# Performance work log

Measured on AMD Instinct MI355X. Metric: run time of the kernel, lower is better.

## Reference

```python
import jax, jax.numpy as jnp
import numpy as np

ALPHA = 0.2  # LeakyReLU negative slope


def setup_inputs() -> dict:
    key = jax.random.key(0)
    k1, k2, k3 = jax.random.split(key, 3)
    B, N, IN, OUT = 64, 2048, 1024, 1024
    features = jax.random.normal(k1, (B, N, IN), dtype=jnp.float32)
    # Xavier-uniform-ish scaling for weights
    W = jax.random.normal(k2, (OUT, IN), dtype=jnp.float32) * (1.0 / np.sqrt(IN))
    w_b = jnp.zeros((OUT,), dtype=jnp.float32)
    a_w = jax.random.normal(k3, (2 * OUT,), dtype=jnp.float32) * (1.0 / np.sqrt(2 * OUT))
    a_b = jnp.zeros((), dtype=jnp.float32)
    bias_out = jnp.zeros((OUT,), dtype=jnp.float32)
    return {"features": features, "W": W, "w_b": w_b, "a_w": a_w, "a_b": a_b, "bias_out": bias_out}


def reference(features, W, w_b, a_w, a_b, bias_out):
    # h = Linear(in_dim, out_dim)(features): [B, N, D]
    h = jnp.einsum('bni,di->bnd', features, W) + w_b
    D = h.shape[-1]
    a1, a2 = a_w[:D], a_w[D:]
    # concat([h_expand, h]) @ a == h[:, :1] . a1 + h . a2  (h_expand broadcasts node 0)
    e = (h[:, 0:1, :] @ a1[:, None]) + jnp.einsum('bnd,d->bn', h, a2)[..., None] + a_b  # [B, N, 1]
    e = jnp.where(e >= 0, e, ALPHA * e)  # LeakyReLU
    attention = jax.nn.softmax(e, axis=1)  # softmax over nodes, [B, N, 1]
    # dropout p=0.0 -> identity
    pooled = jnp.einsum('bnk,bnd->bkd', attention, h)  # [B, 1, D]
    return jax.nn.relu(pooled + bias_out)
```

## Files before the change

kernel.cpp:

```cpp
#include <hip/hip_runtime.h>

#define ALPHA 0.2f
constexpr int B_   = 64;
constexpr int N_   = 2048;
constexpr int IN_  = 1024;
constexpr int OUT_ = 1024;
constexpr int CHUNK = 256;
constexpr int NCH   = N_ / CHUNK;
constexpr int RPW   = CHUNK / 4;

constexpr size_t WA1   = 0;
constexpr size_t WA2   = 1024;
constexpr size_t E0    = 2048;
constexpr size_t ZPART = 2112;
constexpr size_t PART1 = 4096;
constexpr size_t PART2 = 135168;
constexpr size_t GPART = 266240;
constexpr size_t GV    = 790528;

__device__ inline float wave_reduce_sum(float v) {
    #pragma unroll
    for (int off = 32; off > 0; off >>= 1) v += __shfl_xor(v, off);
    return v;
}

__global__ void kW(const float* __restrict__ W, const float* __restrict__ aw,
                   float* __restrict__ ws) {
    int t = threadIdx.x, blk = blockIdx.x;
    float4 acc1 = make_float4(0.f, 0.f, 0.f, 0.f);
    float4 acc2 = make_float4(0.f, 0.f, 0.f, 0.f);
    #pragma unroll
    for (int r = 0; r < 8; ++r) {
        int d = blk * 8 + r;
        float a1 = aw[d], a2 = aw[OUT_ + d];
        float4 w = ((const float4*)(W + (size_t)d * IN_))[t];
        acc1.x += a1 * w.x; acc1.y += a1 * w.y; acc1.z += a1 * w.z; acc1.w += a1 * w.w;
        acc2.x += a2 * w.x; acc2.y += a2 * w.y; acc2.z += a2 * w.z; acc2.w += a2 * w.w;
    }
    ((float4*)(ws + PART1))[blk * 256 + t] = acc1;
    ((float4*)(ws + PART2))[blk * 256 + t] = acc2;
}

__global__ void kS(const float* __restrict__ f, const float* __restrict__ wb,
                   const float* __restrict__ aw, float* __restrict__ ws) {
    int t = threadIdx.x;
    if (blockIdx.x < 8) {
        int idx = blockIdx.x * 256 + t;
        int which = idx >> 10, col = idx & 1023;
        const float* p = ws + (which ? PART2 : PART1) + col;
        float s = 0.f;
        #pragma unroll 8
        for (int r = 0; r < 128; ++r) s += p[(size_t)r * 1024];
        ws[(which ? WA2 : WA1) + col] = s;
    } else {
        int b = blockIdx.x - 8;
        float4 fv = ((const float4*)(f + (size_t)b * N_ * IN_))[t];
        const float4* p1 = (const float4*)(ws + PART1);
        float acc = 0.f;
        #pragma unroll 8
        for (int r = 0; r < 128; ++r) {
            float4 p = p1[(size_t)r * 256 + t];
            acc += fv.x * p.x + fv.y * p.y + fv.z * p.z + fv.w * p.w;
        }
        float4 wbv = ((const float4*)wb)[t];
        float4 a1v = ((const float4*)aw)[t];
        float4 a2v = ((const float4*)(aw + OUT_))[t];
        acc += wbv.x * (a1v.x + a2v.x) + wbv.y * (a1v.y + a2v.y)
             + wbv.z * (a1v.z + a2v.z) + wbv.w * (a1v.w + a2v.w);
        __shared__ float red[256];
        red[t] = acc;
        __syncthreads();
        for (int off = 128; off > 0; off >>= 1) {
            if (t < off) red[t] += red[t + off];
            __syncthreads();
        }
        if (t == 0) ws[E0 + b] = red[0];
    }
}

__global__ void kMain(const float* __restrict__ f, const float* __restrict__ ab,
                      float* __restrict__ ws) {
    int b = blockIdx.y, chunk = blockIdx.x;
    int t = threadIdx.x, wave = t >> 6, lane = t & 63;
    float cst = ws[E0 + b] + ab[0];

    const float4* wa2_4 = (const float4*)(ws + WA2);
    float4 ra2[4];
    #pragma unroll
    for (int k = 0; k < 4; ++k) ra2[k] = wa2_4[k * 64 + lane];

    const float4* fbase = (const float4*)(f + ((size_t)b * N_ + (size_t)chunk * CHUNK) * IN_);
    float4 acc[4];
    #pragma unroll
    for (int k = 0; k < 4; ++k) acc[k] = make_float4(0.f, 0.f, 0.f, 0.f);
    float z = 0.f;

    float4 v[4], nv[4];
    int r = wave;
    #pragma unroll
    for (int k = 0; k < 4; ++k) v[k] = fbase[(size_t)r * 256 + k * 64 + lane];

    for (int i = 0; i < RPW; ++i) {
        int rn = r + 4;
        if (i + 1 < RPW) {
            #pragma unroll
            for (int k = 0; k < 4; ++k) nv[k] = fbase[(size_t)rn * 256 + k * 64 + lane];
        }
        float dot = 0.f;
        #pragma unroll
        for (int k = 0; k < 4; ++k)
            dot += v[k].x * ra2[k].x + v[k].y * ra2[k].y + v[k].z * ra2[k].z + v[k].w * ra2[k].w;
        dot = wave_reduce_sum(dot);
        float e = dot + cst;
        e = e >= 0.f ? e : ALPHA * e;
        float w = __expf(e);
        z += w;
        #pragma unroll
        for (int k = 0; k < 4; ++k) {
            acc[k].x += w * v[k].x; acc[k].y += w * v[k].y;
            acc[k].z += w * v[k].z; acc[k].w += w * v[k].w;
        }
        if (i + 1 < RPW) {
            #pragma unroll
            for (int k = 0; k < 4; ++k) v[k] = nv[k];
        }
        r = rn;
    }

    __shared__ float4 gbuf[4][256];
    __shared__ float  zbuf[4];
    #pragma unroll
    for (int k = 0; k < 4; ++k) gbuf[wave][k * 64 + lane] = acc[k];
    if (lane == 0) zbuf[wave] = z;
    __syncthreads();
    float4 s0 = gbuf[0][t], s1 = gbuf[1][t], s2 = gbuf[2][t], s3 = gbuf[3][t];
    float4 s = make_float4(s0.x + s1.x + s2.x + s3.x, s0.y + s1.y + s2.y + s3.y,
                           s0.z + s1.z + s2.z + s3.z, s0.w + s1.w + s2.w + s3.w);
    ((float4*)(ws + GPART))[((size_t)b * NCH + chunk) * 256 + t] = s;
    if (t == 0) ws[ZPART + b * NCH + chunk] = zbuf[0] + zbuf[1] + zbuf[2] + zbuf[3];
}

__global__ void kE(float* __restrict__ ws) {
    int b = blockIdx.x, t = threadIdx.x;
    __shared__ float zinv;
    if (t == 0) {
        float zz = 0.f;
        #pragma unroll
        for (int c = 0; c < NCH; ++c) zz += ws[ZPART + b * NCH + c];
        zinv = 1.0f / zz;
    }
    __syncthreads();
    const float4* gp = (const float4*)(ws + GPART);
    float4 acc = make_float4(0.f, 0.f, 0.f, 0.f);
    #pragma unroll
    for (int c = 0; c < NCH; ++c) {
        float4 v = gp[((size_t)b * NCH + c) * 256 + t];
        acc.x += v.x; acc.y += v.y; acc.z += v.z; acc.w += v.w;
    }
    acc.x *= zinv; acc.y *= zinv; acc.z *= zinv; acc.w *= zinv;
    ((float4*)(ws + GV))[b * 256 + t] = acc;
}

__global__ void kF(const float* __restrict__ W, const float* __restrict__ wb,
                   const float* __restrict__ bias, const float* __restrict__ ws,
                   float* __restrict__ out) {
    int t = threadIdx.x, wave = t >> 6, lane = t & 63;
    int d  = blockIdx.x * 4 + wave;
    int b0 = blockIdx.y * 32;
    const float4* w4 = (const float4*)(W + (size_t)d * IN_);
    float4 wreg[4];
    #pragma unroll
    for (int k = 0; k < 4; ++k) wreg[k] = w4[k * 64 + lane];
    float wbb = wb[d] + bias[d];
    const float4* gv = (const float4*)(ws + GV);
    #pragma unroll 4
    for (int bi = 0; bi < 32; ++bi) {
        int b = b0 + bi;
        float acc = 0.f;
        #pragma unroll
        for (int k = 0; k < 4; ++k) {
            float4 g = gv[b * 256 + k * 64 + lane];
            acc += g.x * wreg[k].x + g.y * wreg[k].y + g.z * wreg[k].z + g.w * wreg[k].w;
        }
        acc = wave_reduce_sum(acc);
        if (lane == 0) {
            float p = acc + wbb;
            out[(size_t)b * OUT_ + d] = p > 0.f ? p : 0.f;
        }
    }
}

extern "C" void kernel_launch(void* const* d_in, const int* in_sizes, int n_in,
                              void* d_out, int out_size, void* d_ws, size_t ws_size,
                              hipStream_t stream) {
    const float* f    = (const float*)d_in[0];
    const float* W    = (const float*)d_in[1];
    const float* wb   = (const float*)d_in[2];
    const float* aw   = (const float*)d_in[3];
    const float* ab   = (const float*)d_in[4];
    const float* bias = (const float*)d_in[5];
    float* out = (float*)d_out;
    float* ws  = (float*)d_ws;

    kW   <<<dim3(128), 256, 0, stream>>>(W, aw, ws);
    kS   <<<dim3(8 + B_), 256, 0, stream>>>(f, wb, aw, ws);
    kMain<<<dim3(NCH, B_), 256, 0, stream>>>(f, ab, ws);
    kE   <<<dim3(B_), 256, 0, stream>>>(ws);
    kF   <<<dim3(OUT_ / 4, 2), 256, 0, stream>>>(W, wb, bias, ws, out);
}
```

Measured before the change: 129.8 us.

## Fuse W·a projection and node-0 score precompute into one column-split kernel

Replaces the two preprocessing kernels (partial W^T a reductions, then a cross-block sum plus node-0 dot) with a single kernel where each of 64 blocks owns 16 input columns. Each block fully reduces W^T a1 and W^T a2 for its columns and writes partial node-0 scores per batch. The main kernel now sums those 64 partials itself at startup. This removes one launch and the large partial-sum workspace round trip. In exchange, W is read with narrow strided column accesses, and every main-kernel block does a small extra reduction plus a barrier.

```diff
diff --git a/kernel.cpp b/kernel.cpp
--- a/kernel.cpp
+++ b/kernel.cpp
@@ -9,14 +9,11 @@
 constexpr int NCH   = N_ / CHUNK;
 constexpr int RPW   = CHUNK / 4;
 
-constexpr size_t WA1   = 0;
-constexpr size_t WA2   = 1024;
-constexpr size_t E0    = 2048;
-constexpr size_t ZPART = 2112;
-constexpr size_t PART1 = 4096;
-constexpr size_t PART2 = 135168;
-constexpr size_t GPART = 266240;
-constexpr size_t GV    = 790528;
+constexpr size_t WA2   = 0;
+constexpr size_t E0P   = 1024;
+constexpr size_t ZPART = 5120;
+constexpr size_t GPART = 8192;
+constexpr size_t GV    = 532480;
 
 __device__ inline float wave_reduce_sum(float v) {
     #pragma unroll
@@ -24,65 +21,66 @@
     return v;
 }
 
-__global__ void kW(const float* __restrict__ W, const float* __restrict__ aw,
-                   float* __restrict__ ws) {
-    int t = threadIdx.x, blk = blockIdx.x;
-    float4 acc1 = make_float4(0.f, 0.f, 0.f, 0.f);
-    float4 acc2 = make_float4(0.f, 0.f, 0.f, 0.f);
-    #pragma unroll
-    for (int r = 0; r < 8; ++r) {
-        int d = blk * 8 + r;
-        float a1 = aw[d], a2 = aw[OUT_ + d];
-        float4 w = ((const float4*)(W + (size_t)d * IN_))[t];
-        acc1.x += a1 * w.x; acc1.y += a1 * w.y; acc1.z += a1 * w.z; acc1.w += a1 * w.w;
-        acc2.x += a2 * w.x; acc2.y += a2 * w.y; acc2.z += a2 * w.z; acc2.w += a2 * w.w;
-    }
-    ((float4*)(ws + PART1))[blk * 256 + t] = acc1;
-    ((float4*)(ws + PART2))[blk * 256 + t] = acc2;
-}
-
-__global__ void kS(const float* __restrict__ f, const float* __restrict__ wb,
-                   const float* __restrict__ aw, float* __restrict__ ws) {
+__global__ void kPre(const float* __restrict__ W, const float* __restrict__ f,
+                     const float* __restrict__ wb, const float* __restrict__ aw,
+                     float* __restrict__ ws) {
+    int s = blockIdx.x;
     int t = threadIdx.x;
-    if (blockIdx.x < 8) {
-        int idx = blockIdx.x * 256 + t;
-        int which = idx >> 10, col = idx & 1023;
-        const float* p = ws + (which ? PART2 : PART1) + col;
-        float s = 0.f;
-        #pragma unroll 8
-        for (int r = 0; r < 128; ++r) s += p[(size_t)r * 1024];
-        ws[(which ? WA2 : WA1) + col] = s;
-    } else {
-        int b = blockIdx.x - 8;
-        float4 fv = ((const float4*)(f + (size_t)b * N_ * IN_))[t];
-        const float4* p1 = (const float4*)(ws + PART1);
-        float acc = 0.f;
-        #pragma unroll 8
-        for (int r = 0; r < 128; ++r) {
-            float4 p = p1[(size_t)r * 256 + t];
-            acc += fv.x * p.x + fv.y * p.y + fv.z * p.z + fv.w * p.w;
-        }
-        float4 wbv = ((const float4*)wb)[t];
-        float4 a1v = ((const float4*)aw)[t];
-        float4 a2v = ((const float4*)(aw + OUT_))[t];
-        acc += wbv.x * (a1v.x + a2v.x) + wbv.y * (a1v.y + a2v.y)
-             + wbv.z * (a1v.z + a2v.z) + wbv.w * (a1v.w + a2v.w);
-        __shared__ float red[256];
-        red[t] = acc;
-        __syncthreads();
-        for (int off = 128; off > 0; off >>= 1) {
-            if (t < off) red[t] += red[t + off];
-            __syncthreads();
-        }
-        if (t == 0) ws[E0 + b] = red[0];
-    }
+    int c  = t & 15;
+    int rg = t >> 4;
+    int col = s * 16 + c;
+    float a1acc = 0.f, a2acc = 0.f;
+    for (int i = 0; i < 64; ++i) {
+        int d = rg * 64 + i;
+        float w = W[(size_t)d * IN_ + col];
+        a1acc += aw[d] * w;
+        a2acc += aw[OUT_ + d] * w;
+    }
+    __shared__ float s1[16][16], s2[16][16];
+    __shared__ float wa1L[16];
+    __shared__ float wbshare_s;
+    s1[rg][c] = a1acc;
+    s2[rg][c] = a2acc;
+    __syncthreads();
+    if (t < 16) {
+        float x1 = 0.f, x2 = 0.f;
+        #pragma unroll
+        for (int r = 0; r < 16; ++r) { x1 += s1[r][t]; x2 += s2[r][t]; }
+        wa1L[t] = x1;
+        ws[WA2 + s * 16 + t] = x2;
+    }
+    if (t == 0) {
+        float x = 0.f;
+        #pragma unroll
+        for (int c2 = 0; c2 < 16; ++c2) {
+            int cc = s * 16 + c2;
+            x += wb[cc] * (aw[cc] + aw[OUT_ + cc]);
+        }
+        wbshare_s = x;
+    }
+    __syncthreads();
+    int b = t >> 2, q = t & 3;
+    float4 fv = ((const float4*)(f + (size_t)b * N_ * IN_ + s * 16))[q];
+    float4 w1 = ((const float4*)wa1L)[q];
+    float dotv = fv.x * w1.x + fv.y * w1.y + fv.z * w1.z + fv.w * w1.w;
+    dotv += __shfl_xor(dotv, 1);
+    dotv += __shfl_xor(dotv, 2);
+    if (q == 0) ws[E0P + s * 64 + b] = dotv + wbshare_s;
 }
 
 __global__ void kMain(const float* __restrict__ f, const float* __restrict__ ab,
                       float* __restrict__ ws) {
     int b = blockIdx.y, chunk = blockIdx.x;
     int t = threadIdx.x, wave = t >> 6, lane = t & 63;
-    float cst = ws[E0 + b] + ab[0];
+
+    __shared__ float cstS;
+    if (t < 64) {
+        float v = ws[E0P + (size_t)t * 64 + b];
+        v = wave_reduce_sum(v);
+        if (t == 0) cstS = v + ab[0];
+    }
+    __syncthreads();
+    float cst = cstS;
 
     const float4* wa2_4 = (const float4*)(ws + WA2);
     float4 ra2[4];
@@ -202,8 +200,7 @@
     float* out = (float*)d_out;
     float* ws  = (float*)d_ws;
 
-    kW   <<<dim3(128), 256, 0, stream>>>(W, aw, ws);
-    kS   <<<dim3(8 + B_), 256, 0, stream>>>(f, wb, aw, ws);
+    kPre <<<dim3(64), 256, 0, stream>>>(W, f, wb, aw, ws);
     kMain<<<dim3(NCH, B_), 256, 0, stream>>>(f, ab, ws);
     kE   <<<dim3(B_), 256, 0, stream>>>(ws);
     kF   <<<dim3(OUT_ / 4, 2), 256, 0, stream>>>(W, wb, bias, ws, out);
```

Result: faster. 122.3 us (median of 2 runs) (-5.8%).
